# Optimization experiments

Measured on AMD Instinct MI355X. Metric: run time of the kernel, lower is better.

## Reference

```python
import jax, jax.numpy as jnp
import numpy as np

B, C, W, H = 16, 256, 64, 64
D = C // 8  # query/key head dim = 32


def setup_inputs() -> dict:
    key = jax.random.key(0)
    k1, k2, k3 = jax.random.split(key, 3)
    x = jax.random.normal(k1, (B, C, W, H), dtype=jnp.float32)
    # 1x1 conv weights, squeezed to [out_ch, in_ch]
    Wq = jax.random.normal(k2, (D, C), dtype=jnp.float32) * (1.0 / np.sqrt(C))
    Wk = jax.random.normal(k3, (D, C), dtype=jnp.float32) * (1.0 / np.sqrt(C))
    return {"x": x, "Wq": Wq, "Wk": Wk}


def reference(x, Wq, Wk):
    # x: [B, C, W, H]. Attention is row-restricted: independent per (b, w),
    # attending over the H axis. (value_conv in the torch module is unused.)
    q = jnp.einsum('bcwh,dc->bwhd', x, Wq)          # [B, W, H, D]
    k = jnp.einsum('bcwh,dc->bwdh', x, Wk)          # [B, W, D, H]
    energy = jnp.einsum('bwhd,bwdj->bwhj', q, k)    # [B, W, H, H] (unscaled)
    attn = jax.nn.softmax(energy, axis=-1)          # softmax over keys j
    v = jnp.transpose(x, (0, 2, 1, 3))              # [B, W, C, H]
    # torch: bmm(v, attn^T): out[c, i] = sum_j v[c, j] * attn[i, j]
    out = jnp.einsum('bwcj,bwij->bwci', v, attn)    # [B, W, C, H]
    out = jnp.transpose(out, (0, 2, 1, 3))          # [B, C, W, H]
    return out * x                                  # elementwise gate
```

## Files before the change

### kernel.cpp

```cpp
#include <hip/hip_runtime.h>

#define BB 16
#define CCH 256
#define WWD 64
#define HHT 64
#define WH (WWD*HHT)

typedef short bf16x8 __attribute__((ext_vector_type(8)));
typedef float f32x4  __attribute__((ext_vector_type(4)));

__device__ __forceinline__ short f2bf(float f) {
  unsigned u = __builtin_bit_cast(unsigned, f);
  u += 0x7fffu + ((u >> 16) & 1u);
  return (short)(u >> 16);
}
__device__ __forceinline__ float bf2f(short s) {
  unsigned u = ((unsigned)(unsigned short)s) << 16;
  return __builtin_bit_cast(float, u);
}

__global__ __launch_bounds__(256) void selfattn_kernel(
    const float* __restrict__ x, const float* __restrict__ Wq,
    const float* __restrict__ Wk, float* __restrict__ out) {
  __shared__ float    q_lds[64 * 36];
  __shared__ float    k_lds[32 * 64];
  __shared__ unsigned attnT[64 * 64];

  const int tid  = threadIdx.x;
  const int lane = tid & 63;
  const int wave = tid >> 6;
  const int blk  = blockIdx.x;
  const int b    = blk >> 6;
  const int w    = blk & 63;

  const float* xb = x   + (size_t)b * CCH * WH + (size_t)w * HHT;
  float*       ob = out + (size_t)b * CCH * WH + (size_t)w * HHT;

  const int d0 = __builtin_amdgcn_readfirstlane(wave * 8);
  float qa[8] = {0,0,0,0,0,0,0,0};
  float ka[8] = {0,0,0,0,0,0,0,0};
  for (int cb = 0; cb < CCH; cb += 32) {
    float xv[32];
    #pragma unroll
    for (int cc = 0; cc < 32; ++cc) xv[cc] = xb[(size_t)(cb + cc) * WH + lane];
    #pragma unroll
    for (int dd = 0; dd < 8; ++dd) {
      const float4* wq4 = (const float4*)(Wq + (size_t)(d0 + dd) * CCH + cb);
      const float4* wk4 = (const float4*)(Wk + (size_t)(d0 + dd) * CCH + cb);
      float qacc = qa[dd], kacc = ka[dd];
      #pragma unroll
      for (int c4 = 0; c4 < 8; ++c4) {
        const float4 wq = wq4[c4];
        const float4 wk = wk4[c4];
        qacc += xv[4*c4+0]*wq.x + xv[4*c4+1]*wq.y + xv[4*c4+2]*wq.z + xv[4*c4+3]*wq.w;
        kacc += xv[4*c4+0]*wk.x + xv[4*c4+1]*wk.y + xv[4*c4+2]*wk.z + xv[4*c4+3]*wk.w;
      }
      qa[dd] = qacc; ka[dd] = kacc;
    }
  }
  #pragma unroll
  for (int dd = 0; dd < 8; ++dd) {
    q_lds[lane*36 + d0 + dd] = qa[dd];
    k_lds[(d0+dd)*64 + lane] = ka[dd];
  }
  __syncthreads();

  float kc[32];
  #pragma unroll
  for (int d = 0; d < 32; ++d) kc[d] = k_lds[d*64 + lane];

  const int h0 = __builtin_amdgcn_readfirstlane(wave * 16);
  for (int hh = 0; hh < 16; ++hh) {
    const int h = h0 + hh;
    const float4* qrow = (const float4*)&q_lds[h*36];
    float e = 0.f;
    #pragma unroll
    for (int d4 = 0; d4 < 8; ++d4) {
      const float4 qv = qrow[d4];
      e += qv.x*kc[4*d4+0] + qv.y*kc[4*d4+1] + qv.z*kc[4*d4+2] + qv.w*kc[4*d4+3];
    }
    float m = e;
    #pragma unroll
    for (int off = 32; off >= 1; off >>= 1) m = fmaxf(m, __shfl_xor(m, off, 64));
    const float ex = __expf(e - m);
    float s = ex;
    #pragma unroll
    for (int off = 32; off >= 1; off >>= 1) s += __shfl_xor(s, off, 64);
    const float p  = ex / s;
    const short ph = f2bf(p);
    const short pl = f2bf(p - bf2f(ph));
    attnT[lane*64 + (h ^ (lane & 31))] =
        (unsigned)(unsigned short)ph | ((unsigned)(unsigned short)pl << 16);
  }
  __syncthreads();

  const int g   = lane >> 4;
  const int r16 = lane & 15;

  bf16x8 bh[4][2], bl[4][2];
  #pragma unroll
  for (int it = 0; it < 4; ++it) {
    const int i = it*16 + r16;
    #pragma unroll
    for (int ks = 0; ks < 2; ++ks) {
      bf16x8 hfr, lfr;
      #pragma unroll
      for (int t = 0; t < 8; ++t) {
        const int j = ks*32 + g*8 + t;
        const unsigned pw = attnT[j*64 + (i ^ (j & 31))];
        hfr[t] = (short)(pw & 0xffffu);
        lfr[t] = (short)(pw >> 16);
      }
      bh[it][ks] = hfr; bl[it][ks] = lfr;
    }
  }

  const int c0w = __builtin_amdgcn_readfirstlane(wave * 64);
  #pragma unroll
  for (int ct = 0; ct < 4; ++ct) {
    const int crow = c0w + ct*16 + r16;
    bf16x8 xh[2], xl[2];
    #pragma unroll
    for (int ks = 0; ks < 2; ++ks) {
      const float4 f0 = *(const float4*)(xb + (size_t)crow*WH + ks*32 + g*8);
      const float4 f1 = *(const float4*)(xb + (size_t)crow*WH + ks*32 + g*8 + 4);
      const float xs[8] = {f0.x,f0.y,f0.z,f0.w,f1.x,f1.y,f1.z,f1.w};
      bf16x8 hfr, lfr;
      #pragma unroll
      for (int t = 0; t < 8; ++t) {
        hfr[t] = f2bf(xs[t]);
        lfr[t] = f2bf(xs[t] - bf2f(hfr[t]));
      }
      xh[ks] = hfr; xl[ks] = lfr;
    }
    #pragma unroll
    for (int it = 0; it < 4; ++it) {
      f32x4 acc = {0.f, 0.f, 0.f, 0.f};
      #pragma unroll
      for (int ks = 0; ks < 2; ++ks) {
        acc = __builtin_amdgcn_mfma_f32_16x16x32_bf16(xh[ks], bh[it][ks], acc, 0, 0, 0);
        acc = __builtin_amdgcn_mfma_f32_16x16x32_bf16(xh[ks], bl[it][ks], acc, 0, 0, 0);
        acc = __builtin_amdgcn_mfma_f32_16x16x32_bf16(xl[ks], bh[it][ks], acc, 0, 0, 0);
      }
      const int i = it*16 + r16;
      #pragma unroll
      for (int r = 0; r < 4; ++r) {
        const int c = c0w + ct*16 + g*4 + r;
        const float xg = xb[(size_t)c*WH + i];
        ob[(size_t)c*WH + i] = acc[r] * xg;
      }
    }
  }
}

extern "C" void kernel_launch(void* const* d_in, const int* in_sizes, int n_in,
                              void* d_out, int out_size, void* d_ws, size_t ws_size,
                              hipStream_t stream) {
  (void)in_sizes; (void)n_in; (void)d_ws; (void)ws_size; (void)out_size;
  const float* x  = (const float*)d_in[0];
  const float* Wq = (const float*)d_in[1];
  const float* Wk = (const float*)d_in[2];
  float* out = (float*)d_out;
  dim3 grid(BB * WWD);
  dim3 block(256);
  hipLaunchKernelGGL(selfattn_kernel, grid, block, 0, stream, x, Wq, Wk, out);
}
```

Before: 189.3 us.

## Compute Q/K projection with split-bf16 MFMA using pre-split weights, restructure softmax

Adds a small pre-kernel that splits Wq/Wk into hi/lo bf16 MFMA fragments in the workspace. The main kernel then computes the Q/K projection with 3-pass bf16 MFMAs instead of scalar FP32 FMAs. Softmax is reorganised so each wave owns a slice of keys, with max and sum reduced across waves through LDS, and attention is stored in a fragment-friendly layout. The PV stage runs in two halves to cut register pressure, and occupancy is pinned to 4 waves/EU. This adds a second launch and extra barriers, and the bf16 splitting may cost some precision.

```diff
diff --git a/kernel.cpp b/kernel.cpp
--- a/kernel.cpp
+++ b/kernel.cpp
@@ -1,153 +1,212 @@
 #include <hip/hip_runtime.h>
 
-#define BB 16
 #define CCH 256
-#define WWD 64
-#define HHT 64
-#define WH (WWD*HHT)
+#define WH 4096
 
 typedef short bf16x8 __attribute__((ext_vector_type(8)));
 typedef float f32x4  __attribute__((ext_vector_type(4)));
-
-__device__ __forceinline__ short f2bf(float f) {
+typedef unsigned u32x4 __attribute__((ext_vector_type(4)));
+
+__device__ __forceinline__ unsigned f2bf(float f) {
   unsigned u = __builtin_bit_cast(unsigned, f);
   u += 0x7fffu + ((u >> 16) & 1u);
-  return (short)(u >> 16);
-}
-__device__ __forceinline__ float bf2f(short s) {
-  unsigned u = ((unsigned)(unsigned short)s) << 16;
-  return __builtin_bit_cast(float, u);
-}
-
-__global__ __launch_bounds__(256) void selfattn_kernel(
-    const float* __restrict__ x, const float* __restrict__ Wq,
-    const float* __restrict__ Wk, float* __restrict__ out) {
-  __shared__ float    q_lds[64 * 36];
-  __shared__ float    k_lds[32 * 64];
-  __shared__ unsigned attnT[64 * 64];
+  return (u >> 16) & 0xffffu;
+}
+__device__ __forceinline__ float bf2f(unsigned s) {
+  return __builtin_bit_cast(float, s << 16);
+}
+
+__device__ __forceinline__ void split2(float f0, float f1, unsigned& hiw, unsigned& low) {
+  const unsigned u0 = __builtin_bit_cast(unsigned, f0);
+  const unsigned u1 = __builtin_bit_cast(unsigned, f1);
+  hiw = (u0 >> 16) | (u1 & 0xFFFF0000u);
+  const float h0 = __builtin_bit_cast(float, u0 & 0xFFFF0000u);
+  const float h1 = __builtin_bit_cast(float, u1 & 0xFFFF0000u);
+  low = f2bf(f0 - h0) | (f2bf(f1 - h1) << 16);
+}
+
+__global__ __launch_bounds__(256) void wsplit_kernel(
+    const float* __restrict__ Wq, const float* __restrict__ Wk,
+    short* __restrict__ ws) {
+  const int gid    = blockIdx.x * 256 + threadIdx.x;
+  const int fragid = gid >> 6;
+  const int lane   = gid & 63;
+  const int mt = fragid & 3;
+  const int kt = fragid >> 2;
+  const int dp = mt * 16 + (lane & 15);
+  const int cb = kt * 32 + ((lane >> 4) & 3) * 8;
+  const float* Wrow = (dp < 32) ? (Wq + (size_t)dp * CCH)
+                                : (Wk + (size_t)(dp - 32) * CCH);
+  bf16x8 hfr, lfr;
+  #pragma unroll
+  for (int t = 0; t < 8; ++t) {
+    const float v = Wrow[cb + t];
+    const unsigned h = f2bf(v);
+    hfr[t] = (short)h;
+    lfr[t] = (short)f2bf(v - bf2f(h));
+  }
+  *(bf16x8*)(ws + (size_t)gid * 8)         = hfr;
+  *(bf16x8*)(ws + 16384 + (size_t)gid * 8) = lfr;
+}
+
+__global__ __launch_bounds__(256)
+__attribute__((amdgpu_waves_per_eu(4, 4)))
+void selfattn_kernel(
+    const float* __restrict__ x, const short* __restrict__ ws,
+    float* __restrict__ out) {
+  __shared__ float    q_lds[32 * 64];
+  __shared__ float    k_lds[64 * 36];
+  __shared__ unsigned attn32[8 * 8 * 64];
+  __shared__ float    red1[4 * 64];
+  __shared__ float    red2[4 * 64];
 
   const int tid  = threadIdx.x;
   const int lane = tid & 63;
   const int wave = tid >> 6;
+  const int g    = lane >> 4;
+  const int r16  = lane & 15;
   const int blk  = blockIdx.x;
   const int b    = blk >> 6;
   const int w    = blk & 63;
 
-  const float* xb = x   + (size_t)b * CCH * WH + (size_t)w * HHT;
-  float*       ob = out + (size_t)b * CCH * WH + (size_t)w * HHT;
-
-  const int d0 = __builtin_amdgcn_readfirstlane(wave * 8);
-  float qa[8] = {0,0,0,0,0,0,0,0};
-  float ka[8] = {0,0,0,0,0,0,0,0};
-  for (int cb = 0; cb < CCH; cb += 32) {
-    float xv[32];
-    #pragma unroll
-    for (int cc = 0; cc < 32; ++cc) xv[cc] = xb[(size_t)(cb + cc) * WH + lane];
-    #pragma unroll
-    for (int dd = 0; dd < 8; ++dd) {
-      const float4* wq4 = (const float4*)(Wq + (size_t)(d0 + dd) * CCH + cb);
-      const float4* wk4 = (const float4*)(Wk + (size_t)(d0 + dd) * CCH + cb);
-      float qacc = qa[dd], kacc = ka[dd];
-      #pragma unroll
-      for (int c4 = 0; c4 < 8; ++c4) {
-        const float4 wq = wq4[c4];
-        const float4 wk = wk4[c4];
-        qacc += xv[4*c4+0]*wq.x + xv[4*c4+1]*wq.y + xv[4*c4+2]*wq.z + xv[4*c4+3]*wq.w;
-        kacc += xv[4*c4+0]*wk.x + xv[4*c4+1]*wk.y + xv[4*c4+2]*wk.z + xv[4*c4+3]*wk.w;
-      }
-      qa[dd] = qacc; ka[dd] = kacc;
-    }
-  }
-  #pragma unroll
-  for (int dd = 0; dd < 8; ++dd) {
-    q_lds[lane*36 + d0 + dd] = qa[dd];
-    k_lds[(d0+dd)*64 + lane] = ka[dd];
-  }
-  __syncthreads();
-
-  float kc[32];
-  #pragma unroll
-  for (int d = 0; d < 32; ++d) kc[d] = k_lds[d*64 + lane];
-
-  const int h0 = __builtin_amdgcn_readfirstlane(wave * 16);
-  for (int hh = 0; hh < 16; ++hh) {
-    const int h = h0 + hh;
-    const float4* qrow = (const float4*)&q_lds[h*36];
-    float e = 0.f;
+  const float* xb = x   + (size_t)b * CCH * WH + (size_t)w * 64;
+  float*       ob = out + (size_t)b * CCH * WH + (size_t)w * 64;
+
+  {
+    const int col = wave * 16 + r16;
+    f32x4 acc[4] = {{0,0,0,0},{0,0,0,0},{0,0,0,0},{0,0,0,0}};
+    #pragma unroll
+    for (int kt = 0; kt < 8; ++kt) {
+      float xs[8];
+      #pragma unroll
+      for (int t = 0; t < 8; ++t)
+        xs[t] = xb[(size_t)(kt*32 + g*8 + t) * WH + col];
+      unsigned hw[4], lw[4];
+      #pragma unroll
+      for (int r = 0; r < 4; ++r) split2(xs[2*r], xs[2*r+1], hw[r], lw[r]);
+      const bf16x8 xbh = __builtin_bit_cast(bf16x8, (u32x4){hw[0],hw[1],hw[2],hw[3]});
+      const bf16x8 xbl = __builtin_bit_cast(bf16x8, (u32x4){lw[0],lw[1],lw[2],lw[3]});
+      #pragma unroll
+      for (int mt = 0; mt < 4; ++mt) {
+        const bf16x8 ah = *(const bf16x8*)(ws + (size_t)((kt*4 + mt)*64 + lane) * 8);
+        const bf16x8 al = *(const bf16x8*)(ws + 16384 + (size_t)((kt*4 + mt)*64 + lane) * 8);
+        acc[mt] = __builtin_amdgcn_mfma_f32_16x16x32_bf16(ah, xbh, acc[mt], 0, 0, 0);
+        acc[mt] = __builtin_amdgcn_mfma_f32_16x16x32_bf16(ah, xbl, acc[mt], 0, 0, 0);
+        acc[mt] = __builtin_amdgcn_mfma_f32_16x16x32_bf16(al, xbh, acc[mt], 0, 0, 0);
+      }
+    }
+    #pragma unroll
+    for (int mt = 0; mt < 2; ++mt)
+      #pragma unroll
+      for (int r = 0; r < 4; ++r)
+        q_lds[(mt*16 + g*4 + r) * 64 + col] = acc[mt][r];
+    #pragma unroll
+    for (int mt = 2; mt < 4; ++mt)
+      #pragma unroll
+      for (int r = 0; r < 4; ++r)
+        k_lds[col * 36 + (mt-2)*16 + g*4 + r] = acc[mt][r];
+  }
+  __syncthreads();
+
+  float qreg[32];
+  #pragma unroll
+  for (int d = 0; d < 32; ++d) qreg[d] = q_lds[d * 64 + lane];
+
+  float e[16];
+  #pragma unroll
+  for (int jj = 0; jj < 16; ++jj) {
+    const float4* kr = (const float4*)&k_lds[(wave*16 + jj) * 36];
+    float acc = 0.f;
     #pragma unroll
     for (int d4 = 0; d4 < 8; ++d4) {
-      const float4 qv = qrow[d4];
-      e += qv.x*kc[4*d4+0] + qv.y*kc[4*d4+1] + qv.z*kc[4*d4+2] + qv.w*kc[4*d4+3];
-    }
-    float m = e;
-    #pragma unroll
-    for (int off = 32; off >= 1; off >>= 1) m = fmaxf(m, __shfl_xor(m, off, 64));
-    const float ex = __expf(e - m);
-    float s = ex;
-    #pragma unroll
-    for (int off = 32; off >= 1; off >>= 1) s += __shfl_xor(s, off, 64);
-    const float p  = ex / s;
-    const short ph = f2bf(p);
-    const short pl = f2bf(p - bf2f(ph));
-    attnT[lane*64 + (h ^ (lane & 31))] =
-        (unsigned)(unsigned short)ph | ((unsigned)(unsigned short)pl << 16);
-  }
-  __syncthreads();
-
-  const int g   = lane >> 4;
-  const int r16 = lane & 15;
-
-  bf16x8 bh[4][2], bl[4][2];
-  #pragma unroll
-  for (int it = 0; it < 4; ++it) {
-    const int i = it*16 + r16;
-    #pragma unroll
-    for (int ks = 0; ks < 2; ++ks) {
-      bf16x8 hfr, lfr;
-      #pragma unroll
-      for (int t = 0; t < 8; ++t) {
-        const int j = ks*32 + g*8 + t;
-        const unsigned pw = attnT[j*64 + (i ^ (j & 31))];
-        hfr[t] = (short)(pw & 0xffffu);
-        lfr[t] = (short)(pw >> 16);
-      }
-      bh[it][ks] = hfr; bl[it][ks] = lfr;
-    }
-  }
-
-  const int c0w = __builtin_amdgcn_readfirstlane(wave * 64);
-  #pragma unroll
-  for (int ct = 0; ct < 4; ++ct) {
-    const int crow = c0w + ct*16 + r16;
-    bf16x8 xh[2], xl[2];
-    #pragma unroll
-    for (int ks = 0; ks < 2; ++ks) {
-      const float4 f0 = *(const float4*)(xb + (size_t)crow*WH + ks*32 + g*8);
-      const float4 f1 = *(const float4*)(xb + (size_t)crow*WH + ks*32 + g*8 + 4);
-      const float xs[8] = {f0.x,f0.y,f0.z,f0.w,f1.x,f1.y,f1.z,f1.w};
-      bf16x8 hfr, lfr;
-      #pragma unroll
-      for (int t = 0; t < 8; ++t) {
-        hfr[t] = f2bf(xs[t]);
-        lfr[t] = f2bf(xs[t] - bf2f(hfr[t]));
-      }
-      xh[ks] = hfr; xl[ks] = lfr;
-    }
-    #pragma unroll
-    for (int it = 0; it < 4; ++it) {
-      f32x4 acc = {0.f, 0.f, 0.f, 0.f};
+      const float4 kv = kr[d4];
+      acc += qreg[4*d4+0]*kv.x + qreg[4*d4+1]*kv.y
+           + qreg[4*d4+2]*kv.z + qreg[4*d4+3]*kv.w;
+    }
+    e[jj] = acc;
+  }
+  float pm = e[0];
+  #pragma unroll
+  for (int jj = 1; jj < 16; ++jj) pm = fmaxf(pm, e[jj]);
+  red1[wave*64 + lane] = pm;
+  __syncthreads();
+  const float m = fmaxf(fmaxf(red1[lane], red1[64 + lane]),
+                        fmaxf(red1[128 + lane], red1[192 + lane]));
+  float s = 0.f;
+  #pragma unroll
+  for (int jj = 0; jj < 16; ++jj) { e[jj] = __expf(e[jj] - m); s += e[jj]; }
+  red2[wave*64 + lane] = s;
+  __syncthreads();
+  const float stot = (red2[lane] + red2[64 + lane]) + (red2[128 + lane] + red2[192 + lane]);
+  const float rs = 1.0f / stot;
+  {
+    const int fbase = (lane >> 4) * 2 + (wave >> 1);
+    #pragma unroll
+    for (int jj = 0; jj < 16; ++jj) {
+      const float p = e[jj] * rs;
+      const unsigned u = __builtin_bit_cast(unsigned, p);
+      const float hif = __builtin_bit_cast(float, u & 0xFFFF0000u);
+      const unsigned lo = f2bf(p - hif);
+      const int l2 = (((wave & 1) * 2 + (jj >> 3)) << 4) | r16;
+      attn32[fbase*512 + (jj & 7)*64 + l2] = (u >> 16) | (lo << 16);
+    }
+  }
+  __syncthreads();
+
+  const int c0w = wave * 64;
+  #pragma unroll
+  for (int half = 0; half < 2; ++half) {
+    bf16x8 bh[2][2], bl[2][2];
+    #pragma unroll
+    for (int itl = 0; itl < 2; ++itl)
       #pragma unroll
       for (int ks = 0; ks < 2; ++ks) {
-        acc = __builtin_amdgcn_mfma_f32_16x16x32_bf16(xh[ks], bh[it][ks], acc, 0, 0, 0);
-        acc = __builtin_amdgcn_mfma_f32_16x16x32_bf16(xh[ks], bl[it][ks], acc, 0, 0, 0);
-        acc = __builtin_amdgcn_mfma_f32_16x16x32_bf16(xl[ks], bh[it][ks], acc, 0, 0, 0);
-      }
-      const int i = it*16 + r16;
-      #pragma unroll
-      for (int r = 0; r < 4; ++r) {
-        const int c = c0w + ct*16 + g*4 + r;
-        const float xg = xb[(size_t)c*WH + i];
-        ob[(size_t)c*WH + i] = acc[r] * xg;
+        const int f = (half*2 + itl)*2 + ks;
+        unsigned wv[8];
+        #pragma unroll
+        for (int t = 0; t < 8; ++t) wv[t] = attn32[f*512 + t*64 + lane];
+        u32x4 hwv, lwv;
+        #pragma unroll
+        for (int r = 0; r < 4; ++r) {
+          hwv[r] = (wv[2*r] & 0xFFFFu) | (wv[2*r+1] << 16);
+          lwv[r] = (wv[2*r] >> 16)     | (wv[2*r+1] & 0xFFFF0000u);
+        }
+        bh[itl][ks] = __builtin_bit_cast(bf16x8, hwv);
+        bl[itl][ks] = __builtin_bit_cast(bf16x8, lwv);
+      }
+    #pragma unroll
+    for (int ct = 0; ct < 4; ++ct) {
+      const int crow = c0w + ct*16 + r16;
+      const float4* xrow = (const float4*)(xb + (size_t)crow * WH);
+      bf16x8 xh[2], xl[2];
+      #pragma unroll
+      for (int ks = 0; ks < 2; ++ks) {
+        const float4 fa = xrow[ks*8 + g*2];
+        const float4 fb = xrow[ks*8 + g*2 + 1];
+        unsigned hw[4], lw[4];
+        split2(fa.x, fa.y, hw[0], lw[0]);
+        split2(fa.z, fa.w, hw[1], lw[1]);
+        split2(fb.x, fb.y, hw[2], lw[2]);
+        split2(fb.z, fb.w, hw[3], lw[3]);
+        xh[ks] = __builtin_bit_cast(bf16x8, (u32x4){hw[0],hw[1],hw[2],hw[3]});
+        xl[ks] = __builtin_bit_cast(bf16x8, (u32x4){lw[0],lw[1],lw[2],lw[3]});
+      }
+      #pragma unroll
+      for (int itl = 0; itl < 2; ++itl) {
+        f32x4 acc = {0.f, 0.f, 0.f, 0.f};
+        #pragma unroll
+        for (int ks = 0; ks < 2; ++ks) {
+          acc = __builtin_amdgcn_mfma_f32_16x16x32_bf16(xh[ks], bh[itl][ks], acc, 0, 0, 0);
+          acc = __builtin_amdgcn_mfma_f32_16x16x32_bf16(xh[ks], bl[itl][ks], acc, 0, 0, 0);
+          acc = __builtin_amdgcn_mfma_f32_16x16x32_bf16(xl[ks], bh[itl][ks], acc, 0, 0, 0);
+        }
+        const int i = (half*2 + itl)*16 + r16;
+        #pragma unroll
+        for (int r = 0; r < 4; ++r) {
+          const int c = c0w + ct*16 + g*4 + r;
+          const float xg = xb[(size_t)c * WH + i];
+          ob[(size_t)c * WH + i] = acc[r] * xg;
+        }
       }
     }
   }
@@ -156,12 +215,13 @@
 extern "C" void kernel_launch(void* const* d_in, const int* in_sizes, int n_in,
                               void* d_out, int out_size, void* d_ws, size_t ws_size,
                               hipStream_t stream) {
-  (void)in_sizes; (void)n_in; (void)d_ws; (void)ws_size; (void)out_size;
+  (void)in_sizes; (void)n_in; (void)out_size; (void)ws_size;
   const float* x  = (const float*)d_in[0];
   const float* Wq = (const float*)d_in[1];
   const float* Wk = (const float*)d_in[2];
   float* out = (float*)d_out;
-  dim3 grid(BB * WWD);
-  dim3 block(256);
-  hipLaunchKernelGGL(selfattn_kernel, grid, block, 0, stream, x, Wq, Wk, out);
-}
+  hipLaunchKernelGGL(wsplit_kernel, dim3(8), dim3(256), 0, stream,
+                     Wq, Wk, (short*)d_ws);
+  hipLaunchKernelGGL(selfattn_kernel, dim3(16 * 64), dim3(256), 0, stream,
+                     x, (const short*)d_ws, out);
+}
```

Measured after the change: 163.2 us. -13.8%, faster.
